# Kernel optimization log

Measured on AMD Instinct MI355X. Metric: run time of the kernel, lower is better.

## Reference

```python
import jax, jax.numpy as jnp
import numpy as np

DIM = 1024
HEADS = 16
HEAD_DIM = DIM // HEADS

def setup_inputs() -> dict:
    key = jax.random.key(0)
    ks = jax.random.split(key, 6)
    s = 0.02
    return {
        "x": jax.random.normal(ks[0], (2, 2048, DIM), dtype=jnp.float32),
        "w_qkv": jax.random.normal(ks[1], (DIM, 3 * DIM), dtype=jnp.float32) * s,
        "w_proj": jax.random.normal(ks[2], (DIM, DIM), dtype=jnp.float32) * s,
        "b_proj": jnp.zeros((DIM,), dtype=jnp.float32),
        "ln_gamma": jnp.ones((DIM,), dtype=jnp.float32),
        "ln_beta": jnp.zeros((DIM,), dtype=jnp.float32),
    }

def layer_norm(x, gamma, beta, eps=1e-5):
    mu = jnp.mean(x, axis=-1, keepdims=True)
    var = jnp.var(x, axis=-1, keepdims=True)
    return (x - mu) * jax.lax.rsqrt(var + eps) * gamma + beta

def reference(x, w_qkv, w_proj, b_proj, ln_gamma, ln_beta):
    B, N, C = x.shape
    residual = x
    h = layer_norm(x, ln_gamma, ln_beta)
    qkv = h @ w_qkv  # [B,N,3C]
    qkv = qkv.reshape(B, N, 3, HEADS, HEAD_DIM)
    q = jnp.transpose(qkv[:, :, 0], (0, 2, 1, 3))  # [B,H,N,D]
    k = jnp.transpose(qkv[:, :, 1], (0, 2, 1, 3))
    v = jnp.transpose(qkv[:, :, 2], (0, 2, 1, 3))
    scale = 1.0 / jnp.sqrt(jnp.float32(HEAD_DIM))
    attn = jnp.einsum('bhqd,bhkd->bhqk', q, k) * scale
    attn = jax.nn.softmax(attn, axis=-1)
    out = jnp.einsum('bhqk,bhkd->bhqd', attn, v)  # [B,H,N,D]
    out = jnp.transpose(out, (0, 2, 1, 3)).reshape(B, N, C)
    out = out @ w_proj + b_proj
    return out + residual
```

## Files before the change

### kernel.cpp

```cpp
#include <hip/hip_runtime.h>

#define DIM   1024
#define HEADS 16
#define HDIM  64
#define BATCH 2
#define SEQ   2048
#define TOK   (BATCH*SEQ)
#define MEG   1048576

typedef __bf16 bf16x8 __attribute__((ext_vector_type(8)));
typedef float  f32x4  __attribute__((ext_vector_type(4)));
typedef float  f32x16 __attribute__((ext_vector_type(16)));

__device__ __forceinline__ float b2f(ushort u) {
    union { unsigned int u32; float f; } x; x.u32 = ((unsigned int)u) << 16; return x.f;
}
__device__ __forceinline__ ushort f2b(float f) {
    union { float f; unsigned int u32; } x; x.f = f;
    unsigned int r = x.u32 + 0x7FFFu + ((x.u32 >> 16) & 1u);
    return (ushort)(r >> 16);
}
__device__ __forceinline__ void gload_lds16(const ushort* g, void* l) {
    __builtin_amdgcn_global_load_lds((const __attribute__((address_space(1))) void*)g,
                                     (__attribute__((address_space(3))) void*)l, 16, 0, 0);
}
__device__ __forceinline__ float fexp2(float x) {
    float r; asm("v_exp_f32 %0, %1" : "=v"(r) : "v"(x)); return r;
}
__device__ __forceinline__ unsigned int cvtpk_bf16(float lo, float hi) {
    unsigned int r; asm("v_cvt_pk_bf16_f32 %0, %1, %2" : "=v"(r) : "v"(lo), "v"(hi)); return r;
}
__device__ __forceinline__ void plane32swap(unsigned int &a, unsigned int &b) {
    asm("v_permlane32_swap_b32 %0, %1" : "+v"(a), "+v"(b));
}
__device__ __forceinline__ bf16x8 pack8(float e0, float e1, float e2, float e3,
                                        float e4, float e5, float e6, float e7) {
    unsigned int a = cvtpk_bf16(e0, e1), b = cvtpk_bf16(e2, e3);
    unsigned int c = cvtpk_bf16(e4, e5), d = cvtpk_bf16(e6, e7);
    plane32swap(a, c); plane32swap(b, d);
    union { unsigned int u[4]; bf16x8 v; } r;
    r.u[0] = a; r.u[1] = b; r.u[2] = c; r.u[3] = d;
    return r.v;
}

__global__ void transpose_f2b_k(const float* __restrict__ src, ushort* __restrict__ dst,
                                int R, int Cc) {
    __shared__ ushort tile[32][33];
    int c0 = blockIdx.x * 32, r0 = blockIdx.y * 32;
    int tx = threadIdx.x, ty = threadIdx.y;
#pragma unroll
    for (int i = 0; i < 4; i++)
        tile[ty + 8 * i][tx] = f2b(src[(long)(r0 + ty + 8 * i) * Cc + c0 + tx]);
    __syncthreads();
#pragma unroll
    for (int i = 0; i < 4; i++)
        dst[(long)(c0 + ty + 8 * i) * R + r0 + tx] = tile[tx][ty + 8 * i];
}

__global__ __launch_bounds__(256)
void ln_k(const float* __restrict__ x, const float* __restrict__ gamma,
          const float* __restrict__ beta, ushort* __restrict__ h) {
    __shared__ float red[8];
    int row = blockIdx.x, tid = threadIdx.x;
    const float* xr = x + (long)row * DIM;
    float4 xv = *(const float4*)(xr + tid * 4);
    float s1 = xv.x + xv.y + xv.z + xv.w;
    float s2 = xv.x * xv.x + xv.y * xv.y + xv.z * xv.z + xv.w * xv.w;
#pragma unroll
    for (int off = 32; off; off >>= 1) {
        s1 += __shfl_down(s1, off);
        s2 += __shfl_down(s2, off);
    }
    int wid = tid >> 6, lane = tid & 63;
    if (lane == 0) { red[wid * 2] = s1; red[wid * 2 + 1] = s2; }
    __syncthreads();
    s1 = red[0] + red[2] + red[4] + red[6];
    s2 = red[1] + red[3] + red[5] + red[7];
    float mu  = s1 * (1.0f / DIM);
    float var = s2 * (1.0f / DIM) - mu * mu;
    float rs  = rsqrtf(var + 1e-5f);
    float4 gv = *(const float4*)(gamma + tid * 4);
    float4 bv = *(const float4*)(beta + tid * 4);
    ushort4 ov;
    ov.x = f2b((xv.x - mu) * rs * gv.x + bv.x);
    ov.y = f2b((xv.y - mu) * rs * gv.y + bv.y);
    ov.z = f2b((xv.z - mu) * rs * gv.z + bv.z);
    ov.w = f2b((xv.w - mu) * rs * gv.w + bv.w);
    *(ushort4*)(h + (long)row * DIM + tid * 4) = ov;
}

__global__ __launch_bounds__(256, 3)
void gemm_qkv_k(const ushort* __restrict__ A, const ushort* __restrict__ Bt,
                ushort* __restrict__ qp, ushort* __restrict__ kp, ushort* __restrict__ vp) {
    __shared__ __align__(16) ushort smem[17408];
    int tid  = threadIdx.x;
    int wid  = tid >> 6, lane = tid & 63;
    int quad = lane >> 4, l16 = lane & 15;
    int wm = wid >> 1, wn = wid & 1;
    int rowbase = blockIdx.y * 128;
    int colbase = blockIdx.x * 128;

    f32x4 acc[4][4];
#pragma unroll
    for (int i = 0; i < 4; i++)
#pragma unroll
        for (int j = 0; j < 4; j++) acc[i][j] = (f32x4){0.f, 0.f, 0.f, 0.f};

    for (int k0 = 0; k0 < DIM; k0 += 64) {
#pragma unroll
        for (int p = 0; p < 2; p++) {
            int c = wid * 2 + p;
            int r = c * 16 + (lane >> 2);
            int ac = (lane & 3) * 8;
#pragma unroll
            for (int pnl = 0; pnl < 2; pnl++) {
                int cc = k0 + pnl * 32 + ac;
                gload_lds16(A  + (long)(rowbase + r) * DIM + cc,
                            &smem[pnl * 4096 + c * 16 * 32]);
                gload_lds16(Bt + (long)(colbase + r) * DIM + cc,
                            &smem[8192 + pnl * 4096 + c * 16 * 32]);
            }
        }
        __syncthreads();
#pragma unroll
        for (int pnl = 0; pnl < 2; pnl++) {
            bf16x8 fa[4], fb[4];
#pragma unroll
            for (int t = 0; t < 4; t++)
                fa[t] = *(const bf16x8*)(&smem[pnl * 4096 + (wm * 64 + t * 16 + l16) * 32 + quad * 8]);
#pragma unroll
            for (int t = 0; t < 4; t++)
                fb[t] = *(const bf16x8*)(&smem[8192 + pnl * 4096 + (wn * 64 + t * 16 + l16) * 32 + quad * 8]);
#pragma unroll
            for (int i = 0; i < 4; i++)
#pragma unroll
                for (int j = 0; j < 4; j++)
                    acc[i][j] = __builtin_amdgcn_mfma_f32_16x16x32_bf16(fa[i], fb[j], acc[i][j], 0, 0, 0);
        }
        __syncthreads();
    }

    if (colbase >= 2048) {
#pragma unroll
        for (int i = 0; i < 4; i++)
#pragma unroll
            for (int j = 0; j < 4; j++) {
                int cl = wn * 64 + j * 16 + l16;
                int rl = wm * 64 + i * 16 + quad * 4;
#pragma unroll
                for (int r = 0; r < 4; r++)
                    smem[cl * 136 + rl + r] = f2b(acc[i][j][r]);
            }
        __syncthreads();
        int b = rowbase >> 11, nnb = rowbase & 2047;
        int hbase = (colbase - 2048) >> 6;
#pragma unroll
        for (int i = 0; i < 8; i++) {
            int id = i * 256 + tid;
            int cl = id >> 4;
            int off = (id & 15) * 8;
            int hh = hbase + (cl >> 6), d = cl & 63;
            uint4 val = *(const uint4*)(&smem[cl * 136 + off]);
            *(uint4*)(vp + (((long)b * HEADS + hh) * HDIM + d) * SEQ + nnb + off) = val;
        }
    } else {
        float s = (colbase < 1024) ? 0.18033688011f : 1.0f;
#pragma unroll
        for (int i = 0; i < 4; i++)
#pragma unroll
            for (int j = 0; j < 4; j++) {
                int rl = wm * 64 + i * 16 + quad * 4;
                int cl = wn * 64 + j * 16 + l16;
#pragma unroll
                for (int r = 0; r < 4; r++)
                    smem[(rl + r) * 136 + cl] = f2b(acc[i][j][r] * s);
            }
        __syncthreads();
        ushort* dst = (colbase < 1024) ? qp : kp;
        int cb = colbase & 1023;
#pragma unroll
        for (int i = 0; i < 8; i++) {
            int id = i * 256 + tid;
            int rl = id >> 4;
            int ch = id & 15;
            int col = cb + ch * 8;
            int head = col >> 6, d = col & 63;
            int mm = rowbase + rl;
            int b = mm >> 11, nn = mm & 2047;
            uint4 val = *(const uint4*)(&smem[rl * 136 + ch * 8]);
            *(uint4*)(dst + ((((long)b * HEADS + head) * SEQ + nn) << 6) + d) = val;
        }
    }
}

__global__ __launch_bounds__(256, 3)
void gemm_proj_k(const ushort* __restrict__ A, const ushort* __restrict__ Bt,
                 const float* __restrict__ bias, const float* __restrict__ xres,
                 float* __restrict__ outp) {
    __shared__ ushort As[2][128][32];
    __shared__ ushort Bs[2][64][32];
    int tid  = threadIdx.x;
    int wid  = tid >> 6, lane = tid & 63;
    int quad = lane >> 4, l16 = lane & 15;
    int rowbase = blockIdx.y * 128;
    int colbase = blockIdx.x * 64;
    int arow = lane >> 2, acol = (lane & 3) * 8;

    f32x4 acc[2][4];
#pragma unroll
    for (int i = 0; i < 2; i++)
#pragma unroll
        for (int j = 0; j < 4; j++) acc[i][j] = (f32x4){0.f, 0.f, 0.f, 0.f};

    for (int k0 = 0; k0 < DIM; k0 += 64) {
#pragma unroll
        for (int p = 0; p < 2; p++) {
            int c = wid * 2 + p;
            int r = c * 16 + arow;
            int mm = rowbase + r;
            int bq = mm >> 11, nn = mm & 2047;
#pragma unroll
            for (int pnl = 0; pnl < 2; pnl++) {
                int cc = k0 + pnl * 32 + acol;
                int head = cc >> 6, d = cc & 63;
                gload_lds16(A + ((((long)bq * HEADS + head) * SEQ + nn) << 6) + d,
                            &As[pnl][c * 16][0]);
            }
        }
        {
            int r = wid * 16 + arow;
#pragma unroll
            for (int pnl = 0; pnl < 2; pnl++) {
                int cc = k0 + pnl * 32 + acol;
                gload_lds16(Bt + (long)(colbase + r) * DIM + cc, &Bs[pnl][wid * 16][0]);
            }
        }
        __syncthreads();
#pragma unroll
        for (int pnl = 0; pnl < 2; pnl++) {
            bf16x8 fa[2], fb[4];
#pragma unroll
            for (int t = 0; t < 2; t++)
                fa[t] = *(const bf16x8*)(&As[pnl][wid * 32 + t * 16 + l16][quad * 8]);
#pragma unroll
            for (int t = 0; t < 4; t++)
                fb[t] = *(const bf16x8*)(&Bs[pnl][t * 16 + l16][quad * 8]);
#pragma unroll
            for (int i = 0; i < 2; i++)
#pragma unroll
                for (int j = 0; j < 4; j++)
                    acc[i][j] = __builtin_amdgcn_mfma_f32_16x16x32_bf16(fa[i], fb[j], acc[i][j], 0, 0, 0);
        }
        __syncthreads();
    }

#pragma unroll
    for (int i = 0; i < 2; i++)
#pragma unroll
        for (int j = 0; j < 4; j++) {
            int m0  = rowbase + wid * 32 + i * 16 + quad * 4;
            int col = colbase + j * 16 + l16;
#pragma unroll
            for (int r = 0; r < 4; r++) {
                int mm = m0 + r;
                outp[(long)mm * DIM + col] = acc[i][j][r] + bias[col] + xres[(long)mm * DIM + col];
            }
        }
}

__global__ __launch_bounds__(256, 2)
void attn_k(ushort* qio, const ushort* __restrict__ kg,
            const ushort* __restrict__ vt) {
    __shared__ __align__(16) ushort Kp[2][4096];
    __shared__ __align__(16) ushort Vs[2][4096];
    int flat = blockIdx.x;
    int swz  = (flat & 7) * 64 + (flat >> 3);
    int qx = swz & 15, bh = swz >> 4;
    int tid = threadIdx.x, wid = tid >> 6;
    int lane = tid & 63;
    int l31 = lane & 31, hi = lane >> 5;
    ushort* qh = qio + (long)bh * SEQ * HDIM;
    const ushort* kh = kg + (long)bh * SEQ * HDIM;
    const ushort* vh = vt + (long)bh * HDIM * SEQ;

    int srow = tid >> 3, schk = tid & 7;
    int sofs = srow * 64 + ((schk ^ (srow & 7)) * 8);
    const ushort* kbase = kh + (long)srow * HDIM + schk * 8;
    const ushort* vbase = vh + (long)srow * SEQ + schk * 8;

    int qrow0 = qx * 128 + wid * 32;
    bf16x8 qf[4];
#pragma unroll
    for (int ks = 0; ks < 4; ks++)
        qf[ks] = *(const bf16x8*)(qh + (long)(qrow0 + l31) * HDIM + ks * 16 + hi * 8);

    f32x16 o0 = {}, o1 = {};
    f32x4 lac = {0.f, 0.f, 0.f, 0.f};

    uint4 kr0 = *(const uint4*)(kbase);
    uint4 kr1 = *(const uint4*)(kbase + 32 * HDIM);
    uint4 vr0 = *(const uint4*)(vbase);
    uint4 vr1 = *(const uint4*)(vbase + 32 * SEQ);
    *(uint4*)(&Kp[0][sofs])        = kr0;
    *(uint4*)(&Kp[0][sofs + 2048]) = kr1;
    *(uint4*)(&Vs[0][sofs])        = vr0;
    *(uint4*)(&Vs[0][sofs + 2048]) = vr1;

    const int NIT = SEQ / 64;
    for (int it = 0; it < NIT; ++it) {
        int buf = it & 1;
        if (it + 1 < NIT) {
            int kt = (it + 1) * 64;
            kr0 = *(const uint4*)(kbase + (long)kt * HDIM);
            kr1 = *(const uint4*)(kbase + (long)(kt + 32) * HDIM);
            vr0 = *(const uint4*)(vbase + kt);
            vr1 = *(const uint4*)(vbase + 32 * SEQ + kt);
        }
        __syncthreads();

        f32x16 sc0 = {}, sc1 = {};
        __builtin_amdgcn_s_setprio(1);
#pragma unroll
        for (int ks = 0; ks < 4; ks++) {
            int psl = ((2 * ks + hi) ^ (l31 & 7)) * 8;
            bf16x8 ka = *(const bf16x8*)(&Kp[buf][l31 * 64 + psl]);
            bf16x8 kb = *(const bf16x8*)(&Kp[buf][(32 + l31) * 64 + psl]);
            sc0 = __builtin_amdgcn_mfma_f32_32x32x16_bf16(ka, qf[ks], sc0, 0, 0, 0);
            sc1 = __builtin_amdgcn_mfma_f32_32x32x16_bf16(kb, qf[ks], sc1, 0, 0, 0);
        }
        __builtin_amdgcn_s_setprio(0);

        float e0[16], e1[16];
#pragma unroll
        for (int r = 0; r < 16; r++) { e0[r] = fexp2(sc0[r]); e1[r] = fexp2(sc1[r]); }
#pragma unroll
        for (int r = 0; r < 4; r++)
            lac += (f32x4){e0[4*r], e0[4*r+1], e0[4*r+2], e0[4*r+3]}
                 + (f32x4){e1[4*r], e1[4*r+1], e1[4*r+2], e1[4*r+3]};

        bf16x8 pa0 = pack8(e0[0], e0[1], e0[2],  e0[3],  e0[4],  e0[5],  e0[6],  e0[7]);
        bf16x8 pa1 = pack8(e0[8], e0[9], e0[10], e0[11], e0[12], e0[13], e0[14], e0[15]);
        bf16x8 pa2 = pack8(e1[0], e1[1], e1[2],  e1[3],  e1[4],  e1[5],  e1[6],  e1[7]);
        bf16x8 pa3 = pack8(e1[8], e1[9], e1[10], e1[11], e1[12], e1[13], e1[14], e1[15]);

        __builtin_amdgcn_s_setprio(1);
#pragma unroll
        for (int g = 0; g < 4; g++) {
            int psl = ((2 * g + hi) ^ (l31 & 7)) * 8;
            bf16x8 v0 = *(const bf16x8*)(&Vs[buf][l31 * 64 + psl]);
            bf16x8 v1 = *(const bf16x8*)(&Vs[buf][(32 + l31) * 64 + psl]);
            bf16x8 pg = (g == 0) ? pa0 : (g == 1) ? pa1 : (g == 2) ? pa2 : pa3;
            o0 = __builtin_amdgcn_mfma_f32_32x32x16_bf16(pg, v0, o0, 0, 0, 0);
            o1 = __builtin_amdgcn_mfma_f32_32x32x16_bf16(pg, v1, o1, 0, 0, 0);
        }
        __builtin_amdgcn_s_setprio(0);

        if (it + 1 < NIT) {
            *(uint4*)(&Kp[buf ^ 1][sofs])        = kr0;
            *(uint4*)(&Kp[buf ^ 1][sofs + 2048]) = kr1;
            *(uint4*)(&Vs[buf ^ 1][sofs])        = vr0;
            *(uint4*)(&Vs[buf ^ 1][sofs + 2048]) = vr1;
        }
    }

    float t = lac[0] + lac[1] + lac[2] + lac[3];
    t += __shfl_xor(t, 32);
    float linv = 1.0f / t;
#pragma unroll
    for (int r = 0; r < 16; r++) {
        int qrow = (r & 3) + 8 * (r >> 2) + 4 * hi;
        float lr = __shfl(linv, qrow);
        long ro = (long)(qrow0 + qrow) * HDIM;
        qh[ro + l31]      = f2b(o0[r] * lr);
        qh[ro + 32 + l31] = f2b(o1[r] * lr);
    }
}

extern "C" void kernel_launch(void* const* d_in, const int* in_sizes, int n_in,
                              void* d_out, int out_size, void* d_ws, size_t ws_size,
                              hipStream_t stream) {
    const float* x      = (const float*)d_in[0];
    const float* w_qkv  = (const float*)d_in[1];
    const float* w_proj = (const float*)d_in[2];
    const float* b_proj = (const float*)d_in[3];
    const float* gamma  = (const float*)d_in[4];
    const float* beta   = (const float*)d_in[5];
    float* out = (float*)d_out;

    ushort* ws   = (ushort*)d_ws;
    ushort* h    = ws;
    ushort* wqt  = ws + (size_t)4 * MEG;
    ushort* qb   = ws + (size_t)7 * MEG;
    ushort* kb   = ws + (size_t)11 * MEG;
    ushort* vtb  = ws + (size_t)15 * MEG;

    transpose_f2b_k<<<dim3(3 * DIM / 32, DIM / 32), dim3(32, 8), 0, stream>>>(
        w_qkv, wqt, DIM, 3 * DIM);
    ln_k<<<dim3(TOK), dim3(256), 0, stream>>>(x, gamma, beta, h);
    gemm_qkv_k<<<dim3(3 * DIM / 128, TOK / 128), dim3(256), 0, stream>>>(
        h, wqt, qb, kb, vtb);
    attn_k<<<dim3((SEQ / 128) * BATCH * HEADS), dim3(256), 0, stream>>>(qb, kb, vtb);
    transpose_f2b_k<<<dim3(DIM / 32, DIM / 32), dim3(32, 8), 0, stream>>>(
        w_proj, kb, DIM, DIM);
    gemm_proj_k<<<dim3(DIM / 64, TOK / 128), dim3(256), 0, stream>>>(
        qb, kb, b_proj, x, out);
}
```

Before: 183.5 us.

## Restructure QKV GEMM into 256x256 double-buffered tiles with swizzled LDS

The QKV projection GEMM moves from 128x128 tiles with 4 waves to 256x256 tiles with 8 waves. Global-to-LDS loads are double-buffered so the next K-slab streams in while MFMAs run. An XOR swizzle on the LDS layout avoids bank conflicts, and s_setprio is raised around the MFMA bursts. The epilogue writes per-wave patches for the Q/K and transposed-V outputs. Tile reuse per load goes up, but the 128 KB of LDS and larger accumulators cut occupancy, and the grid shrinks to 192 blocks, which may underfill the 256 CUs.

```diff
diff --git a/kernel.cpp b/kernel.cpp
--- a/kernel.cpp
+++ b/kernel.cpp
@@ -89,106 +89,150 @@
     *(ushort4*)(h + (long)row * DIM + tid * 4) = ov;
 }
 
-__global__ __launch_bounds__(256, 3)
+__global__ __launch_bounds__(512, 2)
 void gemm_qkv_k(const ushort* __restrict__ A, const ushort* __restrict__ Bt,
                 ushort* __restrict__ qp, ushort* __restrict__ kp, ushort* __restrict__ vp) {
-    __shared__ __align__(16) ushort smem[17408];
+    __shared__ __align__(16) ushort lds[65536];
     int tid  = threadIdx.x;
     int wid  = tid >> 6, lane = tid & 63;
     int quad = lane >> 4, l16 = lane & 15;
-    int wm = wid >> 1, wn = wid & 1;
-    int rowbase = blockIdx.y * 128;
-    int colbase = blockIdx.x * 128;
-
-    f32x4 acc[4][4];
-#pragma unroll
-    for (int i = 0; i < 4; i++)
+    int wm = wid >> 2, wn = wid & 3;
+    int rowbase = blockIdx.y * 256;
+    int colbase = blockIdx.x * 256;
+    const int NT = DIM / 64;
+
+    f32x4 acc[8][4];
+#pragma unroll
+    for (int i = 0; i < 8; i++)
 #pragma unroll
         for (int j = 0; j < 4; j++) acc[i][j] = (f32x4){0.f, 0.f, 0.f, 0.f};
 
-    for (int k0 = 0; k0 < DIM; k0 += 64) {
-#pragma unroll
-        for (int p = 0; p < 2; p++) {
-            int c = wid * 2 + p;
-            int r = c * 16 + (lane >> 2);
-            int ac = (lane & 3) * 8;
-#pragma unroll
-            for (int pnl = 0; pnl < 2; pnl++) {
-                int cc = k0 + pnl * 32 + ac;
-                gload_lds16(A  + (long)(rowbase + r) * DIM + cc,
-                            &smem[pnl * 4096 + c * 16 * 32]);
-                gload_lds16(Bt + (long)(colbase + r) * DIM + cc,
-                            &smem[8192 + pnl * 4096 + c * 16 * 32]);
-            }
-        }
-        __syncthreads();
-#pragma unroll
-        for (int pnl = 0; pnl < 2; pnl++) {
-            bf16x8 fa[4], fb[4];
-#pragma unroll
-            for (int t = 0; t < 4; t++)
-                fa[t] = *(const bf16x8*)(&smem[pnl * 4096 + (wm * 64 + t * 16 + l16) * 32 + quad * 8]);
-#pragma unroll
-            for (int t = 0; t < 4; t++)
-                fb[t] = *(const bf16x8*)(&smem[8192 + pnl * 4096 + (wn * 64 + t * 16 + l16) * 32 + quad * 8]);
-#pragma unroll
-            for (int i = 0; i < 4; i++)
-#pragma unroll
-                for (int j = 0; j < 4; j++)
-                    acc[i][j] = __builtin_amdgcn_mfma_f32_16x16x32_bf16(fa[i], fb[j], acc[i][j], 0, 0, 0);
-        }
-        __syncthreads();
-    }
-
-    if (colbase >= 2048) {
-#pragma unroll
-        for (int i = 0; i < 4; i++)
-#pragma unroll
-            for (int j = 0; j < 4; j++) {
-                int cl = wn * 64 + j * 16 + l16;
-                int rl = wm * 64 + i * 16 + quad * 4;
-#pragma unroll
-                for (int r = 0; r < 4; r++)
-                    smem[cl * 136 + rl + r] = f2b(acc[i][j][r]);
-            }
-        __syncthreads();
-        int b = rowbase >> 11, nnb = rowbase & 2047;
-        int hbase = (colbase - 2048) >> 6;
-#pragma unroll
-        for (int i = 0; i < 8; i++) {
-            int id = i * 256 + tid;
-            int cl = id >> 4;
-            int off = (id & 15) * 8;
-            int hh = hbase + (cl >> 6), d = cl & 63;
-            uint4 val = *(const uint4*)(&smem[cl * 136 + off]);
-            *(uint4*)(vp + (((long)b * HEADS + hh) * HDIM + d) * SEQ + nnb + off) = val;
+#pragma unroll
+    for (int i = 0; i < 8; ++i) {
+        int seg = wid * 4096 + i * 512;
+        int o = seg + lane * 8;
+        if (seg < 16384) {
+            int row = o >> 6, p = (o >> 3) & 7, c = p ^ (row & 7);
+            gload_lds16(A + (long)(rowbase + row) * DIM + c * 8, lds + seg);
+        } else {
+            int o2 = o - 16384;
+            int row = o2 >> 6, p = (o2 >> 3) & 7, c = p ^ (row & 7);
+            gload_lds16(Bt + (long)(colbase + row) * DIM + c * 8,
+                        lds + 32768 + (seg - 16384));
+        }
+    }
+    asm volatile("s_waitcnt vmcnt(0)" ::: "memory");
+    __syncthreads();
+
+    for (int t = 0; t < NT; ++t) {
+        const ushort* Ab = lds + (t & 1) * 16384;
+        const ushort* Bb = lds + 32768 + (t & 1) * 16384;
+        if (t + 1 < NT) {
+            int k0n = (t + 1) * 64;
+            ushort* dA = lds + ((t + 1) & 1) * 16384;
+            ushort* dB = lds + 32768 + ((t + 1) & 1) * 16384;
+#pragma unroll
+            for (int i = 0; i < 8; ++i) {
+                int seg = wid * 4096 + i * 512;
+                int o = seg + lane * 8;
+                if (seg < 16384) {
+                    int row = o >> 6, p = (o >> 3) & 7, c = p ^ (row & 7);
+                    gload_lds16(A + (long)(rowbase + row) * DIM + k0n + c * 8, dA + seg);
+                } else {
+                    int o2 = o - 16384;
+                    int row = o2 >> 6, p = (o2 >> 3) & 7, c = p ^ (row & 7);
+                    gload_lds16(Bt + (long)(colbase + row) * DIM + k0n + c * 8,
+                                dB + (seg - 16384));
+                }
+            }
+        }
+        bf16x8 fb[4];
+#pragma unroll
+        for (int ph = 0; ph < 4; ++ph) {
+            int rh = ph & 1, ks = ph >> 1;
+            if (rh == 0) {
+#pragma unroll
+                for (int j = 0; j < 4; ++j) {
+                    int row = wn * 64 + j * 16 + l16;
+                    int p = (ks * 4 + quad) ^ (row & 7);
+                    fb[j] = *(const bf16x8*)(Bb + row * 64 + p * 8);
+                }
+            }
+            bf16x8 fa[4];
+#pragma unroll
+            for (int i = 0; i < 4; ++i) {
+                int row = wm * 128 + rh * 64 + i * 16 + l16;
+                int p = (ks * 4 + quad) ^ (row & 7);
+                fa[i] = *(const bf16x8*)(Ab + row * 64 + p * 8);
+            }
+            asm volatile("" ::: "memory");
+            __builtin_amdgcn_s_barrier();
+            __builtin_amdgcn_s_setprio(1);
+#pragma unroll
+            for (int i = 0; i < 4; ++i)
+#pragma unroll
+                for (int j = 0; j < 4; ++j)
+                    acc[rh * 4 + i][j] = __builtin_amdgcn_mfma_f32_16x16x32_bf16(
+                        fa[i], fb[j], acc[rh * 4 + i][j], 0, 0, 0);
+            __builtin_amdgcn_s_setprio(0);
+            if (ph == 3) asm volatile("s_waitcnt vmcnt(0)" ::: "memory");
+            asm volatile("" ::: "memory");
+            __builtin_amdgcn_s_barrier();
+        }
+    }
+    __syncthreads();
+
+    ushort* patch = lds + wid * 4608;
+    int col0 = colbase + wn * 64;
+    int part = col0 >> 10;
+    int head = (col0 & 1023) >> 6;
+    if (part < 2) {
+        ushort* dst = (part == 0) ? qp : kp;
+        float s = (part == 0) ? 0.18033688011f : 1.0f;
+#pragma unroll
+        for (int rh = 0; rh < 2; ++rh) {
+#pragma unroll
+            for (int i = 0; i < 4; ++i)
+#pragma unroll
+                for (int j = 0; j < 4; ++j)
+#pragma unroll
+                    for (int r = 0; r < 4; ++r)
+                        patch[(i * 16 + quad * 4 + r) * 72 + j * 16 + l16] =
+                            f2b(acc[rh * 4 + i][j][r] * s);
+            asm volatile("s_waitcnt lgkmcnt(0)" ::: "memory");
+#pragma unroll
+            for (int sf = 0; sf < 8; ++sf) {
+                int row = sf * 8 + (lane >> 3);
+                int ch  = lane & 7;
+                int token = rowbase + wm * 128 + rh * 64 + row;
+                int b = token >> 11, nn = token & 2047;
+                uint4 v = *(const uint4*)(patch + row * 72 + ch * 8);
+                *(uint4*)(dst + ((((long)b * HEADS + head) * SEQ + nn) << 6) + ch * 8) = v;
+            }
+            asm volatile("s_waitcnt lgkmcnt(0)" ::: "memory");
         }
     } else {
-        float s = (colbase < 1024) ? 0.18033688011f : 1.0f;
-#pragma unroll
-        for (int i = 0; i < 4; i++)
-#pragma unroll
-            for (int j = 0; j < 4; j++) {
-                int rl = wm * 64 + i * 16 + quad * 4;
-                int cl = wn * 64 + j * 16 + l16;
-#pragma unroll
-                for (int r = 0; r < 4; r++)
-                    smem[(rl + r) * 136 + cl] = f2b(acc[i][j][r] * s);
-            }
-        __syncthreads();
-        ushort* dst = (colbase < 1024) ? qp : kp;
-        int cb = colbase & 1023;
-#pragma unroll
-        for (int i = 0; i < 8; i++) {
-            int id = i * 256 + tid;
-            int rl = id >> 4;
-            int ch = id & 15;
-            int col = cb + ch * 8;
-            int head = col >> 6, d = col & 63;
-            int mm = rowbase + rl;
-            int b = mm >> 11, nn = mm & 2047;
-            uint4 val = *(const uint4*)(&smem[rl * 136 + ch * 8]);
-            *(uint4*)(dst + ((((long)b * HEADS + head) * SEQ + nn) << 6) + d) = val;
+#pragma unroll
+        for (int th = 0; th < 2; ++th) {
+#pragma unroll
+            for (int i = 0; i < 4; ++i)
+#pragma unroll
+                for (int j = 0; j < 4; ++j)
+#pragma unroll
+                    for (int r = 0; r < 4; ++r)
+                        patch[(j * 16 + l16) * 72 + i * 16 + quad * 4 + r] =
+                            f2b(acc[th * 4 + i][j][r]);
+            asm volatile("s_waitcnt lgkmcnt(0)" ::: "memory");
+            int token0 = rowbase + wm * 128 + th * 64;
+            int b = token0 >> 11, nnb = token0 & 2047;
+#pragma unroll
+            for (int sf = 0; sf < 8; ++sf) {
+                int d  = sf * 8 + (lane >> 3);
+                int ch = lane & 7;
+                uint4 v = *(const uint4*)(patch + d * 72 + ch * 8);
+                *(uint4*)(vp + (((long)b * HEADS + head) * HDIM + d) * SEQ + nnb + ch * 8) = v;
+            }
+            asm volatile("s_waitcnt lgkmcnt(0)" ::: "memory");
         }
     }
 }
@@ -397,7 +441,7 @@
     transpose_f2b_k<<<dim3(3 * DIM / 32, DIM / 32), dim3(32, 8), 0, stream>>>(
         w_qkv, wqt, DIM, 3 * DIM);
     ln_k<<<dim3(TOK), dim3(256), 0, stream>>>(x, gamma, beta, h);
-    gemm_qkv_k<<<dim3(3 * DIM / 128, TOK / 128), dim3(256), 0, stream>>>(
+    gemm_qkv_k<<<dim3(3 * DIM / 256, TOK / 256), dim3(512), 0, stream>>>(
         h, wqt, qb, kb, vtb);
     attn_k<<<dim3((SEQ / 128) * BATCH * HEADS), dim3(256), 0, stream>>>(qb, kb, vtb);
     transpose_f2b_k<<<dim3(DIM / 32, DIM / 32), dim3(32, 8), 0, stream>>>(
```

Result: no change. 185.6 us (+1.2%).

## Split KV sequence across two wave groups per attention block and merge

Applied to the files above, without the earlier changes.

The attention block now has 512 threads in two groups of four waves. Each group covers the same 128 query rows but only half of the key/value sequence, with its own double-buffered LDS region. After the loop, the second group writes its partial output and row sums to LDS and the first group adds them before normalising and storing. This doubles the waves per CU to better hide latency on the exp/MFMA chain, at the cost of more LDS per block, an extra reduction step and extra block-wide barriers.

```diff
diff --git a/kernel.cpp b/kernel.cpp
--- a/kernel.cpp
+++ b/kernel.cpp
@@ -268,27 +268,33 @@
         }
 }
 
-__global__ __launch_bounds__(256, 2)
+__global__ __launch_bounds__(512, 4)
 void attn_k(ushort* qio, const ushort* __restrict__ kg,
             const ushort* __restrict__ vt) {
-    __shared__ __align__(16) ushort Kp[2][4096];
-    __shared__ __align__(16) ushort Vs[2][4096];
+    __shared__ __align__(16) ushort lds[32768];
     int flat = blockIdx.x;
     int swz  = (flat & 7) * 64 + (flat >> 3);
     int qx = swz & 15, bh = swz >> 4;
-    int tid = threadIdx.x, wid = tid >> 6;
+    int tid = threadIdx.x;
+    int wid = tid >> 6;
+    int qw  = wid & 3;
+    int kvh = wid >> 2;
     int lane = tid & 63;
     int l31 = lane & 31, hi = lane >> 5;
     ushort* qh = qio + (long)bh * SEQ * HDIM;
-    const ushort* kh = kg + (long)bh * SEQ * HDIM;
-    const ushort* vh = vt + (long)bh * HDIM * SEQ;
-
-    int srow = tid >> 3, schk = tid & 7;
+    const ushort* kh = kg + (long)bh * SEQ * HDIM + (long)kvh * 1024 * HDIM;
+    const ushort* vh = vt + (long)bh * HDIM * SEQ + kvh * 1024;
+
+    ushort* Kp = lds + kvh * 16384;
+    ushort* Vs = lds + kvh * 16384 + 8192;
+
+    int gtid = tid & 255;
+    int srow = gtid >> 3, schk = gtid & 7;
     int sofs = srow * 64 + ((schk ^ (srow & 7)) * 8);
     const ushort* kbase = kh + (long)srow * HDIM + schk * 8;
     const ushort* vbase = vh + (long)srow * SEQ + schk * 8;
 
-    int qrow0 = qx * 128 + wid * 32;
+    int qrow0 = qx * 128 + qw * 32;
     bf16x8 qf[4];
 #pragma unroll
     for (int ks = 0; ks < 4; ks++)
@@ -301,14 +307,14 @@
     uint4 kr1 = *(const uint4*)(kbase + 32 * HDIM);
     uint4 vr0 = *(const uint4*)(vbase);
     uint4 vr1 = *(const uint4*)(vbase + 32 * SEQ);
-    *(uint4*)(&Kp[0][sofs])        = kr0;
-    *(uint4*)(&Kp[0][sofs + 2048]) = kr1;
-    *(uint4*)(&Vs[0][sofs])        = vr0;
-    *(uint4*)(&Vs[0][sofs + 2048]) = vr1;
-
-    const int NIT = SEQ / 64;
+    *(uint4*)(Kp + sofs)        = kr0;
+    *(uint4*)(Kp + sofs + 2048) = kr1;
+    *(uint4*)(Vs + sofs)        = vr0;
+    *(uint4*)(Vs + sofs + 2048) = vr1;
+
+    const int NIT = 1024 / 64;
     for (int it = 0; it < NIT; ++it) {
-        int buf = it & 1;
+        int bofs = (it & 1) * 4096;
         if (it + 1 < NIT) {
             int kt = (it + 1) * 64;
             kr0 = *(const uint4*)(kbase + (long)kt * HDIM);
@@ -323,8 +329,8 @@
 #pragma unroll
         for (int ks = 0; ks < 4; ks++) {
             int psl = ((2 * ks + hi) ^ (l31 & 7)) * 8;
-            bf16x8 ka = *(const bf16x8*)(&Kp[buf][l31 * 64 + psl]);
-            bf16x8 kb = *(const bf16x8*)(&Kp[buf][(32 + l31) * 64 + psl]);
+            bf16x8 ka = *(const bf16x8*)(Kp + bofs + l31 * 64 + psl);
+            bf16x8 kb = *(const bf16x8*)(Kp + bofs + (32 + l31) * 64 + psl);
             sc0 = __builtin_amdgcn_mfma_f32_32x32x16_bf16(ka, qf[ks], sc0, 0, 0, 0);
             sc1 = __builtin_amdgcn_mfma_f32_32x32x16_bf16(kb, qf[ks], sc1, 0, 0, 0);
         }
@@ -347,8 +353,8 @@
 #pragma unroll
         for (int g = 0; g < 4; g++) {
             int psl = ((2 * g + hi) ^ (l31 & 7)) * 8;
-            bf16x8 v0 = *(const bf16x8*)(&Vs[buf][l31 * 64 + psl]);
-            bf16x8 v1 = *(const bf16x8*)(&Vs[buf][(32 + l31) * 64 + psl]);
+            bf16x8 v0 = *(const bf16x8*)(Vs + bofs + l31 * 64 + psl);
+            bf16x8 v1 = *(const bf16x8*)(Vs + bofs + (32 + l31) * 64 + psl);
             bf16x8 pg = (g == 0) ? pa0 : (g == 1) ? pa1 : (g == 2) ? pa2 : pa3;
             o0 = __builtin_amdgcn_mfma_f32_32x32x16_bf16(pg, v0, o0, 0, 0, 0);
             o1 = __builtin_amdgcn_mfma_f32_32x32x16_bf16(pg, v1, o1, 0, 0, 0);
@@ -356,23 +362,40 @@
         __builtin_amdgcn_s_setprio(0);
 
         if (it + 1 < NIT) {
-            *(uint4*)(&Kp[buf ^ 1][sofs])        = kr0;
-            *(uint4*)(&Kp[buf ^ 1][sofs + 2048]) = kr1;
-            *(uint4*)(&Vs[buf ^ 1][sofs])        = vr0;
-            *(uint4*)(&Vs[buf ^ 1][sofs + 2048]) = vr1;
+            int nofs = (it & 1) ^ 1 ? 4096 : 4096;
+            nofs = ((it + 1) & 1) * 4096;
+            *(uint4*)(Kp + nofs + sofs)        = kr0;
+            *(uint4*)(Kp + nofs + sofs + 2048) = kr1;
+            *(uint4*)(Vs + nofs + sofs)        = vr0;
+            *(uint4*)(Vs + nofs + sofs + 2048) = vr1;
         }
     }
 
     float t = lac[0] + lac[1] + lac[2] + lac[3];
     t += __shfl_xor(t, 32);
-    float linv = 1.0f / t;
-#pragma unroll
-    for (int r = 0; r < 16; r++) {
-        int qrow = (r & 3) + 8 * (r >> 2) + 4 * hi;
-        float lr = __shfl(linv, qrow);
-        long ro = (long)(qrow0 + qrow) * HDIM;
-        qh[ro + l31]      = f2b(o0[r] * lr);
-        qh[ro + 32 + l31] = f2b(o1[r] * lr);
+    __syncthreads();
+    float* cb = (float*)lds;
+    if (kvh == 1) {
+        float* my = cb + (qw * 64 + lane) * 34;
+#pragma unroll
+        for (int r = 0; r < 16; r++) { my[r] = o0[r]; my[16 + r] = o1[r]; }
+        my[32] = t;
+    }
+    __syncthreads();
+    if (kvh == 0) {
+        const float* ot = cb + (qw * 64 + lane) * 34;
+#pragma unroll
+        for (int r = 0; r < 16; r++) { o0[r] += ot[r]; o1[r] += ot[16 + r]; }
+        t += ot[32];
+        float linv = 1.0f / t;
+#pragma unroll
+        for (int r = 0; r < 16; r++) {
+            int qrow = (r & 3) + 8 * (r >> 2) + 4 * hi;
+            float lr = __shfl(linv, qrow);
+            long ro = (long)(qrow0 + qrow) * HDIM;
+            qh[ro + l31]      = f2b(o0[r] * lr);
+            qh[ro + 32 + l31] = f2b(o1[r] * lr);
+        }
     }
 }
 
@@ -399,7 +422,7 @@
     ln_k<<<dim3(TOK), dim3(256), 0, stream>>>(x, gamma, beta, h);
     gemm_qkv_k<<<dim3(3 * DIM / 128, TOK / 128), dim3(256), 0, stream>>>(
         h, wqt, qb, kb, vtb);
-    attn_k<<<dim3((SEQ / 128) * BATCH * HEADS), dim3(256), 0, stream>>>(qb, kb, vtb);
+    attn_k<<<dim3((SEQ / 128) * BATCH * HEADS), dim3(512), 0, stream>>>(qb, kb, vtb);
     transpose_f2b_k<<<dim3(DIM / 32, DIM / 32), dim3(32, 8), 0, stream>>>(
         w_proj, kb, DIM, DIM);
     gemm_proj_k<<<dim3(DIM / 64, TOK / 128), dim3(256), 0, stream>>>(
```

Result: slower. 195.5 us (+6.5%).
